# Optimization experiments

Hardware: AMD Instinct MI355X
Metric: run time of the kernel (lower is better)

## Reference

```python
import jax, jax.numpy as jnp
import numpy as np

ALPHA = 2
BETA = 4
# np.finfo(float64).eps threshold used in gaussian2D (max is always 1.0 at center)
EPS64 = 2.220446049250313e-16
CLIP = 1e-4


def _splat_level(boxes, labels, B, C, H, W):
    # boxes: [B,N,4] normalized cxcywh; labels: [B,N] int class ids
    # centers/radius in feature coordinates (scale_x*orig_w cancels to W)
    x = jnp.floor(boxes[..., 0] * W).astype(jnp.int32)           # [B,N]
    y = jnp.floor(boxes[..., 1] * H).astype(jnp.int32)
    bw = boxes[..., 2] * W
    bh = boxes[..., 3] * H
    r = jnp.maximum(1, jnp.floor((bw + bh) / 4.0).astype(jnp.int32))  # int() truncation, positive -> floor
    sigma = (2 * r + 1).astype(jnp.float32) / 6.0                # sigma = diameter/6

    dx = jnp.arange(W, dtype=jnp.int32)[None, None, :] - x[..., None]   # [B,N,W]
    dy = jnp.arange(H, dtype=jnp.int32)[None, None, :] - y[..., None]   # [B,N,H]
    d2 = (dx * dx)[:, :, None, :] + (dy * dy)[:, :, :, None]            # [B,N,H,W]
    g = jnp.exp(-d2.astype(jnp.float32) / (2.0 * sigma * sigma)[..., None, None])
    # window |d|<=r (border clipping is implicit since pixels lie in [0,W)x[0,H))
    inwin = (jnp.abs(dx) <= r[..., None])[:, :, None, :] & (jnp.abs(dy) <= r[..., None])[:, :, :, None]
    g = jnp.where(inwin & (g >= EPS64), g, 0.0)

    # scatter-max per (batch, label) channel
    N = boxes.shape[1]
    sid = (labels.astype(jnp.int32) + C * jnp.arange(B, dtype=jnp.int32)[:, None]).reshape(-1)  # [B*N]
    tm = jax.ops.segment_max(g.reshape(B * N, H * W), sid, num_segments=B * C)
    return jnp.maximum(tm, 0.0).reshape(B, C, H * W)  # empty segments (-inf) -> 0 init


def _forward(h0, h1, h2, boxes, labels):
    B, C = h0.shape[0], h0.shape[1]
    bx = jax.lax.stop_gradient(boxes)  # target construction is non-differentiable in the original
    maps = [h0, h1, h2]
    target = jnp.concatenate([_splat_level(bx, labels, B, C, m.shape[-2], m.shape[-1]) for m in maps], axis=2)
    heat = jnp.concatenate([m.reshape(B, C, -1) for m in maps], axis=2)

    pos = (target == 1.0).astype(heat.dtype)
    neg = (target < 1.0).astype(heat.dtype)
    neg_w = jnp.power(1.0 - target, BETA)
    p = jnp.clip(jax.nn.sigmoid(heat), CLIP, 1.0 - CLIP)
    pos_loss = jnp.log(p) * jnp.power(1.0 - p, ALPHA) * pos
    neg_loss = jnp.log(1.0 - p) * jnp.power(p, ALPHA) * neg_w * neg

    num_pos = pos.sum(axis=2, keepdims=True)
    pl = pos_loss.sum(axis=2, keepdims=True)
    nl = neg_loss.sum(axis=2, keepdims=True)
    safe = jnp.where(num_pos == 0, 1.0, num_pos)
    loss = jnp.where(num_pos == 0, -nl, -(pl + nl) / safe)
    loss = jnp.minimum(loss, 10.0)
    lm = jnp.log1p(loss.mean())
    return lm / (1.0 + lm)


def setup_inputs() -> dict:
    key = jax.random.key(0)
    k0, k1, k2, kb, kl = jax.random.split(key, 5)
    B, N, C = 8, 32, 80
    heat_map0 = jax.random.normal(k0, (B, C, 128, 128), dtype=jnp.float32)
    heat_map1 = jax.random.normal(k1, (B, C, 64, 64), dtype=jnp.float32)
    heat_map2 = jax.random.normal(k2, (B, C, 32, 32), dtype=jnp.float32)
    u = jax.random.uniform(kb, (B, N, 4), dtype=jnp.float32)
    boxes = jnp.concatenate([0.05 + 0.9 * u[..., :2], 0.02 + 0.4 * u[..., 2:]], axis=-1)
    labels = jax.random.randint(kl, (B, N), 0, C, dtype=jnp.int32)
    image_sizes = jnp.full((B, 2), 1024, dtype=jnp.int64)
    return {"heat_map0": heat_map0, "heat_map1": heat_map1, "heat_map2": heat_map2,
            "boxes": boxes, "labels": labels, "image_sizes": image_sizes}


def reference(heat_map0, heat_map1, heat_map2, boxes, labels, image_sizes):
    # image_sizes cancels out in the original math (scale_x * orig_w == feature W)
    return _forward(heat_map0, heat_map1, heat_map2, boxes, labels)
```

## Files before the change

kernel.cpp:

```cpp
#include <hip/hip_runtime.h>


#define BATCH 8
#define NBOX 32
#define NCH 80
#define NPLANE 640

__device__ __forceinline__ float sigclip(float h) {
    const float e = __expf(-h);
    const float p = __builtin_amdgcn_rcpf(1.0f + e);
    return fminf(fmaxf(p, 1e-4f), 1.0f - 1e-4f);
}
__device__ __forceinline__ float negterm(float h) {
    const float p = sigclip(h);
    return __logf(1.0f - p) * p * p;
}

__global__ __launch_bounds__(256) void hough_main_kernel(
    const float* __restrict__ h0, const float* __restrict__ h1,
    const float* __restrict__ h2,
    const float* __restrict__ boxes, const int* __restrict__ labels,
    float* __restrict__ ws)
{
    const int bid = blockIdx.x;
    const int tid = threadIdx.x;

    if (bid >= 256) {
        const int p = bid - 256;
        float nl = 0.0f;
        {
            const float4* f4 = (const float4*)(h0 + ((size_t)p << 14));
            for (int i = tid; i < 4096; i += 256) {
                const float4 q = f4[i];
                nl += negterm(q.x) + negterm(q.y) + negterm(q.z) + negterm(q.w);
            }
        }
        {
            const float4* f4 = (const float4*)(h1 + ((size_t)p << 12));
            for (int i = tid; i < 1024; i += 256) {
                const float4 q = f4[i];
                nl += negterm(q.x) + negterm(q.y) + negterm(q.z) + negterm(q.w);
            }
        }
        {
            const float4* f4 = (const float4*)(h2 + ((size_t)p << 10));
            for (int i = tid; i < 256; i += 256) {
                const float4 q = f4[i];
                nl += negterm(q.x) + negterm(q.y) + negterm(q.z) + negterm(q.w);
            }
        }
        for (int o = 32; o > 0; o >>= 1) nl += __shfl_down(nl, o, 64);
        __shared__ float sw[4];
        const int w = tid >> 6, l = tid & 63;
        if (l == 0) sw[w] = nl;
        __syncthreads();
        if (tid == 0) ws[p] = sw[0] + sw[1] + sw[2] + sw[3];
        return;
    }

    const int box = bid;
    const int b = box >> 5, n = box & 31;

    __shared__ int   s_lab[NBOX];
    __shared__ int   s_xm[3][NBOX], s_ym[3][NBOX], s_rm[3][NBOX];
    __shared__ float s_i2[3][NBOX];
    __shared__ int   s_cand[NBOX];
    __shared__ int   s_kc;
    if (tid < NBOX) s_lab[tid] = labels[b * NBOX + tid];
    if (tid < 3 * NBOX) {
        const int lv = tid >> 5, m = tid & 31;
        const float fW = (float)(1 << (7 - lv));
        const float* bp = boxes + (size_t)(b * NBOX + m) * 4;
        s_xm[lv][m] = (int)floorf(bp[0] * fW);
        s_ym[lv][m] = (int)floorf(bp[1] * fW);
        int r = (int)floorf((bp[2] * fW + bp[3] * fW) * 0.25f);
        r = max(1, r);
        s_rm[lv][m] = r;
        const float sig = (float)(2 * r + 1) / 6.0f;
        s_i2[lv][m] = 1.0f / (2.0f * sig * sig);
    }
    __syncthreads();
    const int c = s_lab[n];
    if (tid == 0) {
        int kc = 0;
        for (int m = 0; m < NBOX; ++m)
            if (s_lab[m] == c) s_cand[kc++] = m;
        s_kc = kc;
    }
    __syncthreads();
    const int kc = s_kc;

    float np_ = 0.0f, pl_ = 0.0f, nld = 0.0f;
    const float* heats[3] = {h0, h1, h2};

    for (int lv = 0; lv < 3; ++lv) {
        const int lw = 7 - lv;
        const int W = 1 << lw;
        const int xn = s_xm[lv][n], yn = s_ym[lv][n], rn = s_rm[lv][n];
        const int wn = 2 * rn + 1;
        const int tot = wn * wn;
        const float inv_wn = __builtin_amdgcn_rcpf((float)wn);
        const float* hb = heats[lv] + ((size_t)(b * NCH + c) << (2 * lw));

        for (int idx = tid; idx < tot; idx += 256) {
            int dy = (int)((float)idx * inv_wn);
            int rem = idx - dy * wn;
            if (rem < 0)        { dy -= 1; rem += wn; }
            else if (rem >= wn) { dy += 1; rem -= wn; }
            const int px = xn - rn + rem;
            const int py = yn - rn + dy;
            if (px < 0 || px >= W || py < 0 || py >= W) continue;

            bool owned = true;
            float t = 0.0f;
            for (int j = 0; j < kc; ++j) {
                const int m = s_cand[j];
                const int rm = s_rm[lv][m];
                const int ddx = px - s_xm[lv][m], ddy = py - s_ym[lv][m];
                if (ddx < -rm || ddx > rm || ddy < -rm || ddy > rm) continue;
                if (m < n) { owned = false; break; }
                t = fmaxf(t, __expf(-(float)(ddx * ddx + ddy * ddy) * s_i2[lv][m]));
            }
            if (!owned) continue;

            const float h = hb[py * W + px];
            const float n0 = negterm(h);
            if (t == 1.0f) {
                const float p = sigclip(h);
                const float omp = 1.0f - p;
                pl_ += __logf(p) * omp * omp;
                np_ += 1.0f;
                nld -= n0;
            } else {
                const float omt = 1.0f - t;
                const float nw4 = (omt * omt) * (omt * omt);
                nld += n0 * (nw4 - 1.0f);
            }
        }
    }

    for (int o = 32; o > 0; o >>= 1) {
        np_ += __shfl_down(np_, o, 64);
        pl_ += __shfl_down(pl_, o, 64);
        nld += __shfl_down(nld, o, 64);
    }
    __shared__ float r_np[4], r_pl[4], r_nl[4];
    const int w = tid >> 6, l = tid & 63;
    if (l == 0) { r_np[w] = np_; r_pl[w] = pl_; r_nl[w] = nld; }
    __syncthreads();
    if (tid == 0) {
        ws[640 + box]  = r_np[0] + r_np[1] + r_np[2] + r_np[3];
        ws[896 + box]  = r_pl[0] + r_pl[1] + r_pl[2] + r_pl[3];
        ws[1152 + box] = r_nl[0] + r_nl[1] + r_nl[2] + r_nl[3];
    }
}

__global__ __launch_bounds__(256) void finalize_kernel(
    const float* __restrict__ ws, const int* __restrict__ labels,
    float* __restrict__ out)
{
    const int tid = threadIdx.x;
    float s = 0.0f;
    for (int p = tid; p < NPLANE; p += 256) {
        const int b = p / NCH, c = p - b * NCH;
        float nl = ws[p];
        float np_ = 0.0f, pl_ = 0.0f;
        for (int m = 0; m < NBOX; ++m) {
            if (labels[b * NBOX + m] == c) {
                const int box = b * NBOX + m;
                np_ += ws[640 + box];
                pl_ += ws[896 + box];
                nl  += ws[1152 + box];
            }
        }
        const float loss = (np_ == 0.0f) ? (-nl) : (-(pl_ + nl) / np_);
        s += fminf(loss, 10.0f);
    }
    for (int o = 32; o > 0; o >>= 1) s += __shfl_down(s, o, 64);
    __shared__ float sw[4];
    const int w = tid >> 6, l = tid & 63;
    if (l == 0) sw[w] = s;
    __syncthreads();
    if (tid == 0) {
        const float mean = (sw[0] + sw[1] + sw[2] + sw[3]) * (1.0f / (float)NPLANE);
        const float lm = log1pf(mean);
        out[0] = lm / (1.0f + lm);
    }
}

extern "C" void kernel_launch(void* const* d_in, const int* in_sizes, int n_in,
                              void* d_out, int out_size, void* d_ws, size_t ws_size,
                              hipStream_t stream) {
    const float* h0 = (const float*)d_in[0];
    const float* h1 = (const float*)d_in[1];
    const float* h2 = (const float*)d_in[2];
    const float* boxes = (const float*)d_in[3];
    const int* labels = (const int*)d_in[4];

    float* ws = (float*)d_ws;

    hough_main_kernel<<<896, 256, 0, stream>>>(h0, h1, h2, boxes, labels, ws);
    finalize_kernel<<<1, 256, 0, stream>>>(ws, labels, (float*)d_out);
}
```

Baseline: 118.2 us.

## Split dense and per-box work into finer blocks across levels and plane chunks

The dense negative-term reduction is now split into 4096-element chunks, so each h0 plane uses four blocks and h1 and h2 planes use one block each. That raises the block count from 640 to 3840. The per-box correction work is also split per pyramid level, giving 768 blocks instead of 256. The aim is better load balance and occupancy across the GPU's compute units, since each old block did a long serial loop. The finalize kernel now sums more partial slots, and each box block recomputes its shared setup once per level.

```diff
diff --git a/kernel.cpp b/kernel.cpp
--- a/kernel.cpp
+++ b/kernel.cpp
@@ -5,6 +5,8 @@
 #define NBOX 32
 #define NCH 80
 #define NPLANE 640
+#define NB_B 768
+#define GRID (NB_B + 3840)
 
 __device__ __forceinline__ float sigclip(float h) {
     const float e = __expf(-h);
@@ -25,59 +27,53 @@
     const int bid = blockIdx.x;
     const int tid = threadIdx.x;
 
-    if (bid >= 256) {
-        const int p = bid - 256;
+    if (bid >= NB_B) {
+        const int aid = bid - NB_B;
+        const float* hp; int nf4;
+        if (aid < 2560) {
+            hp = h0 + ((size_t)aid << 12); nf4 = 1024;
+        } else if (aid < 3200) {
+            hp = h1 + ((size_t)(aid - 2560) << 12); nf4 = 1024;
+        } else {
+            hp = h2 + ((size_t)(aid - 3200) << 10); nf4 = 256;
+        }
+        const float4* f4 = (const float4*)hp;
         float nl = 0.0f;
-        {
-            const float4* f4 = (const float4*)(h0 + ((size_t)p << 14));
-            for (int i = tid; i < 4096; i += 256) {
-                const float4 q = f4[i];
-                nl += negterm(q.x) + negterm(q.y) + negterm(q.z) + negterm(q.w);
-            }
-        }
-        {
-            const float4* f4 = (const float4*)(h1 + ((size_t)p << 12));
-            for (int i = tid; i < 1024; i += 256) {
-                const float4 q = f4[i];
-                nl += negterm(q.x) + negterm(q.y) + negterm(q.z) + negterm(q.w);
-            }
-        }
-        {
-            const float4* f4 = (const float4*)(h2 + ((size_t)p << 10));
-            for (int i = tid; i < 256; i += 256) {
-                const float4 q = f4[i];
-                nl += negterm(q.x) + negterm(q.y) + negterm(q.z) + negterm(q.w);
-            }
+        for (int i = tid; i < nf4; i += 256) {
+            const float4 q = f4[i];
+            nl += negterm(q.x) + negterm(q.y) + negterm(q.z) + negterm(q.w);
         }
         for (int o = 32; o > 0; o >>= 1) nl += __shfl_down(nl, o, 64);
         __shared__ float sw[4];
         const int w = tid >> 6, l = tid & 63;
         if (l == 0) sw[w] = nl;
         __syncthreads();
-        if (tid == 0) ws[p] = sw[0] + sw[1] + sw[2] + sw[3];
+        if (tid == 0) ws[aid] = sw[0] + sw[1] + sw[2] + sw[3];
         return;
     }
 
-    const int box = bid;
+    const int lv = bid >> 8;
+    const int box = bid & 255;
     const int b = box >> 5, n = box & 31;
+    const int lw = 7 - lv;
+    const int W = 1 << lw;
+    const float fW = (float)W;
 
     __shared__ int   s_lab[NBOX];
-    __shared__ int   s_xm[3][NBOX], s_ym[3][NBOX], s_rm[3][NBOX];
-    __shared__ float s_i2[3][NBOX];
+    __shared__ int   s_xm[NBOX], s_ym[NBOX], s_rm[NBOX];
+    __shared__ float s_i2[NBOX];
     __shared__ int   s_cand[NBOX];
     __shared__ int   s_kc;
-    if (tid < NBOX) s_lab[tid] = labels[b * NBOX + tid];
-    if (tid < 3 * NBOX) {
-        const int lv = tid >> 5, m = tid & 31;
-        const float fW = (float)(1 << (7 - lv));
-        const float* bp = boxes + (size_t)(b * NBOX + m) * 4;
-        s_xm[lv][m] = (int)floorf(bp[0] * fW);
-        s_ym[lv][m] = (int)floorf(bp[1] * fW);
+    if (tid < NBOX) {
+        s_lab[tid] = labels[b * NBOX + tid];
+        const float* bp = boxes + (size_t)(b * NBOX + tid) * 4;
+        s_xm[tid] = (int)floorf(bp[0] * fW);
+        s_ym[tid] = (int)floorf(bp[1] * fW);
         int r = (int)floorf((bp[2] * fW + bp[3] * fW) * 0.25f);
         r = max(1, r);
-        s_rm[lv][m] = r;
+        s_rm[tid] = r;
         const float sig = (float)(2 * r + 1) / 6.0f;
-        s_i2[lv][m] = 1.0f / (2.0f * sig * sig);
+        s_i2[tid] = 1.0f / (2.0f * sig * sig);
     }
     __syncthreads();
     const int c = s_lab[n];
@@ -90,52 +86,47 @@
     __syncthreads();
     const int kc = s_kc;
 
+    const int xn = s_xm[n], yn = s_ym[n], rn = s_rm[n];
+    const int wn = 2 * rn + 1;
+    const int tot = wn * wn;
+    const float inv_wn = __builtin_amdgcn_rcpf((float)wn);
+    const float* hb = ((lv == 0) ? h0 : (lv == 1) ? h1 : h2)
+                      + ((size_t)(b * NCH + c) << (2 * lw));
+
     float np_ = 0.0f, pl_ = 0.0f, nld = 0.0f;
-    const float* heats[3] = {h0, h1, h2};
-
-    for (int lv = 0; lv < 3; ++lv) {
-        const int lw = 7 - lv;
-        const int W = 1 << lw;
-        const int xn = s_xm[lv][n], yn = s_ym[lv][n], rn = s_rm[lv][n];
-        const int wn = 2 * rn + 1;
-        const int tot = wn * wn;
-        const float inv_wn = __builtin_amdgcn_rcpf((float)wn);
-        const float* hb = heats[lv] + ((size_t)(b * NCH + c) << (2 * lw));
-
-        for (int idx = tid; idx < tot; idx += 256) {
-            int dy = (int)((float)idx * inv_wn);
-            int rem = idx - dy * wn;
-            if (rem < 0)        { dy -= 1; rem += wn; }
-            else if (rem >= wn) { dy += 1; rem -= wn; }
-            const int px = xn - rn + rem;
-            const int py = yn - rn + dy;
-            if (px < 0 || px >= W || py < 0 || py >= W) continue;
-
-            bool owned = true;
-            float t = 0.0f;
-            for (int j = 0; j < kc; ++j) {
-                const int m = s_cand[j];
-                const int rm = s_rm[lv][m];
-                const int ddx = px - s_xm[lv][m], ddy = py - s_ym[lv][m];
-                if (ddx < -rm || ddx > rm || ddy < -rm || ddy > rm) continue;
-                if (m < n) { owned = false; break; }
-                t = fmaxf(t, __expf(-(float)(ddx * ddx + ddy * ddy) * s_i2[lv][m]));
-            }
-            if (!owned) continue;
-
-            const float h = hb[py * W + px];
-            const float n0 = negterm(h);
-            if (t == 1.0f) {
-                const float p = sigclip(h);
-                const float omp = 1.0f - p;
-                pl_ += __logf(p) * omp * omp;
-                np_ += 1.0f;
-                nld -= n0;
-            } else {
-                const float omt = 1.0f - t;
-                const float nw4 = (omt * omt) * (omt * omt);
-                nld += n0 * (nw4 - 1.0f);
-            }
+    for (int idx = tid; idx < tot; idx += 256) {
+        int dy = (int)((float)idx * inv_wn);
+        int rem = idx - dy * wn;
+        if (rem < 0)        { dy -= 1; rem += wn; }
+        else if (rem >= wn) { dy += 1; rem -= wn; }
+        const int px = xn - rn + rem;
+        const int py = yn - rn + dy;
+        if (px < 0 || px >= W || py < 0 || py >= W) continue;
+
+        bool owned = true;
+        float t = 0.0f;
+        for (int j = 0; j < kc; ++j) {
+            const int m = s_cand[j];
+            const int rm = s_rm[m];
+            const int ddx = px - s_xm[m], ddy = py - s_ym[m];
+            if (ddx < -rm || ddx > rm || ddy < -rm || ddy > rm) continue;
+            if (m < n) { owned = false; break; }
+            t = fmaxf(t, __expf(-(float)(ddx * ddx + ddy * ddy) * s_i2[m]));
+        }
+        if (!owned) continue;
+
+        const float h = hb[py * W + px];
+        const float n0 = negterm(h);
+        if (t == 1.0f) {
+            const float p = sigclip(h);
+            const float omp = 1.0f - p;
+            pl_ += __logf(p) * omp * omp;
+            np_ += 1.0f;
+            nld -= n0;
+        } else {
+            const float omt = 1.0f - t;
+            const float nw4 = (omt * omt) * (omt * omt);
+            nld += n0 * (nw4 - 1.0f);
         }
     }
 
@@ -149,9 +140,10 @@
     if (l == 0) { r_np[w] = np_; r_pl[w] = pl_; r_nl[w] = nld; }
     __syncthreads();
     if (tid == 0) {
-        ws[640 + box]  = r_np[0] + r_np[1] + r_np[2] + r_np[3];
-        ws[896 + box]  = r_pl[0] + r_pl[1] + r_pl[2] + r_pl[3];
-        ws[1152 + box] = r_nl[0] + r_nl[1] + r_nl[2] + r_nl[3];
+        const int slot = lv * 256 + box;
+        ws[3840 + slot] = r_np[0] + r_np[1] + r_np[2] + r_np[3];
+        ws[4608 + slot] = r_pl[0] + r_pl[1] + r_pl[2] + r_pl[3];
+        ws[5376 + slot] = r_nl[0] + r_nl[1] + r_nl[2] + r_nl[3];
     }
 }
 
@@ -163,14 +155,19 @@
     float s = 0.0f;
     for (int p = tid; p < NPLANE; p += 256) {
         const int b = p / NCH, c = p - b * NCH;
-        float nl = ws[p];
+        const float4 n4 = ((const float4*)ws)[p];
+        float nl = n4.x + n4.y + n4.z + n4.w + ws[2560 + p] + ws[3200 + p];
         float np_ = 0.0f, pl_ = 0.0f;
         for (int m = 0; m < NBOX; ++m) {
             if (labels[b * NBOX + m] == c) {
                 const int box = b * NBOX + m;
-                np_ += ws[640 + box];
-                pl_ += ws[896 + box];
-                nl  += ws[1152 + box];
+                #pragma unroll
+                for (int lv = 0; lv < 3; ++lv) {
+                    const int slot = lv * 256 + box;
+                    np_ += ws[3840 + slot];
+                    pl_ += ws[4608 + slot];
+                    nl  += ws[5376 + slot];
+                }
             }
         }
         const float loss = (np_ == 0.0f) ? (-nl) : (-(pl_ + nl) / np_);
@@ -199,6 +196,6 @@
 
     float* ws = (float*)d_ws;
 
-    hough_main_kernel<<<896, 256, 0, stream>>>(h0, h1, h2, boxes, labels, ws);
+    hough_main_kernel<<<GRID, 256, 0, stream>>>(h0, h1, h2, boxes, labels, ws);
     finalize_kernel<<<1, 256, 0, stream>>>(ws, labels, (float*)d_out);
 }
```

Result: faster. 115.0 us (-2.8%).
